# Optimization experiments

Hardware: AMD Instinct MI355X
Metric: run time of the kernel (lower is better)

The kernel has to match this reference:

```python
import jax, jax.numpy as jnp
import numpy as np

B, N, H = 512, 100, 768
I = 2 * H  # intermediate_dim default = hidden_dim * 2
NUM_ANS = 16
MAX_ANS = 15
LN_EPS = 1e-5


def setup_inputs() -> dict:
    key = jax.random.key(0)
    ks = jax.random.split(key, 7)
    s = 0.02
    return {
        "v_emb": jax.random.normal(ks[0], (B, N, H), dtype=jnp.float32),
        "W1": jax.random.normal(ks[1], (H, I), dtype=jnp.float32) * s,
        "b1": jax.random.normal(ks[2], (I,), dtype=jnp.float32) * s,
        "gamma": jnp.ones((I,), dtype=jnp.float32),
        "beta": jnp.zeros((I,), dtype=jnp.float32),
        "W2": jax.random.normal(ks[3], (I, 1), dtype=jnp.float32) * s,
        "b2": jax.random.normal(ks[4], (1,), dtype=jnp.float32) * s,
    }


def reference(v_emb, W1, b1, gamma, beta, W2, b2):
    # Linear -> GELU (exact/erf, torch nn.GELU default) -> LayerNorm -> Linear
    h = jnp.einsum("bnh,hi->bni", v_emb, W1) + b1            # [B,N,I]
    h = jax.nn.gelu(h, approximate=False)
    mu = jnp.mean(h, axis=-1, keepdims=True)
    var = jnp.mean(jnp.square(h - mu), axis=-1, keepdims=True)
    h = (h - mu) * jax.lax.rsqrt(var + LN_EPS) * gamma + beta
    scores = jnp.einsum("bni,io->bno", h, W2) + b2           # [B,N,1]
    scores = jax.nn.sigmoid(scores)                           # sigmoid=True branch
    pred = jnp.sum(scores, axis=1)                            # [B,1]
    # pred_to_logits: vectorized round + clamp + one-hot scatter
    # str(int(round(p))) in {'0'..'15'} -> that id; negative -> 0; overflow -> max_ans
    aid = jnp.clip(jnp.round(pred[:, 0]).astype(jnp.int32), 0, MAX_ANS)
    logits = jax.nn.one_hot(aid, NUM_ANS, dtype=scores.dtype)  # [B,16]
    # original returns dict: scores, final_attention_map (==scores), pred, logits
    return scores, pred, logits
```

## Files before the change

kernel.cpp:

```cpp
#include <hip/hip_runtime.h>
#include <hip/hip_bf16.h>
#include <cstdint>
#include <cstddef>

#define BB   512
#define NN   100
#define HH   768
#define II   1536
#define MM   (BB*NN)

typedef __bf16 bf16;
typedef __bf16 bf16x4 __attribute__((ext_vector_type(4)));
typedef __bf16 bf16x8 __attribute__((ext_vector_type(8)));
typedef float  f32x4  __attribute__((ext_vector_type(4)));

__device__ __forceinline__ void gld_lds16(const bf16* g, bf16* l) {
    __builtin_amdgcn_global_load_lds(
        (const __attribute__((address_space(1))) void*)g,
        (__attribute__((address_space(3))) void*)l, 16, 0, 0);
}

__device__ __forceinline__ float fast_gelu(float x) {
    const float ax = fabsf(x) * 0.70710678118654752f;
    const float t  = __builtin_amdgcn_rcpf(fmaf(0.3275911f, ax, 1.0f));
    float p = fmaf(1.061405429f, t, -1.453152027f);
    p = fmaf(p, t, 1.421413741f);
    p = fmaf(p, t, -0.284496736f);
    p = fmaf(p, t, 0.254829592f);
    p = p * t;
    const float e    = __expf(-ax * ax);
    const float erfa = fmaf(-p, e, 1.0f);
    const float erfx = copysignf(erfa, x);
    return 0.5f * x * (1.0f + erfx);
}

__global__ __launch_bounds__(256) void prep_kernel(
    const float* __restrict__ W1, const float* __restrict__ gamma,
    const float* __restrict__ beta, const float* __restrict__ W2,
    const float* __restrict__ b2,
    bf16* __restrict__ Wp, float* __restrict__ gw, float* __restrict__ scal)
{
    int bid = blockIdx.x;
    if (bid < 1152) {
        int t  = bid * 256 + threadIdx.x;
        int n  = t % II;
        int k0 = (t / II) * 4;
        bf16x4 v;
        v[0] = (bf16)W1[(size_t)(k0+0)*II + n];
        v[1] = (bf16)W1[(size_t)(k0+1)*II + n];
        v[2] = (bf16)W1[(size_t)(k0+2)*II + n];
        v[3] = (bf16)W1[(size_t)(k0+3)*II + n];
        *(bf16x4*)&Wp[(size_t)n*HH + k0] = v;
    } else if (bid == 1152) {
        for (int j = threadIdx.x; j < II; j += 256)
            gw[j] = gamma[j] * W2[j];
    } else {
        float s1 = 0.f, s2 = 0.f;
        for (int j = threadIdx.x; j < II; j += 256) {
            float w2 = W2[j];
            s1 += gamma[j] * w2;
            s2 += beta[j]  * w2;
        }
        #pragma unroll
        for (int off = 32; off; off >>= 1) {
            s1 += __shfl_down(s1, off, 64);
            s2 += __shfl_down(s2, off, 64);
        }
        __shared__ float a1[4], a2[4];
        int lane = threadIdx.x & 63, w = threadIdx.x >> 6;
        if (lane == 0) { a1[w] = s1; a2[w] = s2; }
        __syncthreads();
        if (threadIdx.x == 0) {
            scal[0] = a1[0] + a1[1] + a1[2] + a1[3];
            scal[1] = a2[0] + a2[1] + a2[2] + a2[3] + b2[0];
        }
    }
}

__global__ __launch_bounds__(256) void conv_kernel(
    const float* __restrict__ A, bf16* __restrict__ Apk)
{
    const size_t i = ((size_t)blockIdx.x * 256 + threadIdx.x) * 4;
    float4 v = *(const float4*)&A[i];
    bf16x4 o = { (bf16)v.x, (bf16)v.y, (bf16)v.z, (bf16)v.w };
    *(bf16x4*)&Apk[i] = o;
}

__global__ __launch_bounds__(256) void gemm_part(
    const bf16* __restrict__ Apk, const bf16* __restrict__ Wp,
    const float* __restrict__ b1, const float* __restrict__ gw,
    float* __restrict__ part)
{
    __shared__ bf16  As[128 * 64];
    __shared__ bf16  Bs[128 * 64];
    __shared__ float sred[2][128][3];

    const int tid  = threadIdx.x;
    const int lin  = (blockIdx.x % 8) * 600 + blockIdx.x / 8;
    const int mb   = lin / 12;
    const int nb   = lin % 12;
    const int lane = tid & 63;
    const int w    = tid >> 6;
    const int wm   = w >> 1;
    const int wn   = w & 1;
    const int m15  = lane & 15;
    const int q    = lane >> 4;
    const int row0 = mb * 128;

    const int rsub = tid >> 3;
    const int kgA  = (tid & 7) ^ (rsub & 7);
    const size_t gbase = (size_t)rsub * HH + (size_t)kgA * 8;
    const int    lbase = tid * 8;

    const bf16* Ag = Apk + (size_t)row0 * HH;
    const bf16* Bg = Wp  + (size_t)(nb * 128) * HH;

    f32x4 acc[4][4] = {};

    for (int kt = 0; kt < 12; ++kt) {
        const int koff = kt * 64;
        #pragma unroll
        for (int it = 0; it < 4; ++it) {
            size_t go = gbase + (size_t)it * 32 * HH + koff;
            int    lo = lbase + it * 2048;
            gld_lds16(Ag + go, &As[lo]);
            gld_lds16(Bg + go, &Bs[lo]);
        }
        asm volatile("s_waitcnt vmcnt(0)" ::: "memory");
        __syncthreads();

        #pragma unroll
        for (int kb = 0; kb < 2; ++kb) {
            const int swz = (((kb * 4 + q) ^ (m15 & 7)) * 8);
            bf16x8 af[4], bfr[4];
            #pragma unroll
            for (int mt = 0; mt < 4; ++mt)
                af[mt] = *(const bf16x8*)&As[(wm*64 + mt*16 + m15) * 64 + swz];
            #pragma unroll
            for (int nt = 0; nt < 4; ++nt)
                bfr[nt] = *(const bf16x8*)&Bs[(wn*64 + nt*16 + m15) * 64 + swz];
            #pragma unroll
            for (int mt = 0; mt < 4; ++mt)
                #pragma unroll
                for (int nt = 0; nt < 4; ++nt)
                    acc[mt][nt] = __builtin_amdgcn_mfma_f32_16x16x32_bf16(
                        af[mt], bfr[nt], acc[mt][nt], 0, 0, 0);
        }
        __syncthreads();
    }

    float bv[4], gv[4];
    #pragma unroll
    for (int nt = 0; nt < 4; ++nt) {
        const int col = nb*128 + wn*64 + nt*16 + m15;
        bv[nt] = b1[col];
        gv[nt] = gw[col];
    }

    #pragma unroll
    for (int mt = 0; mt < 4; ++mt) {
        #pragma unroll
        for (int r = 0; r < 4; ++r) {
            float x0 = 0.f, x1 = 0.f, x2 = 0.f;
            #pragma unroll
            for (int nt = 0; nt < 4; ++nt) {
                float g = fast_gelu(acc[mt][nt][r] + bv[nt]);
                x0 += g; x1 += g * g; x2 += g * gv[nt];
            }
            #pragma unroll
            for (int off = 8; off; off >>= 1) {
                x0 += __shfl_down(x0, off, 16);
                x1 += __shfl_down(x1, off, 16);
                x2 += __shfl_down(x2, off, 16);
            }
            if (m15 == 0) {
                const int rl = wm*64 + mt*16 + q*4 + r;
                sred[wn][rl][0] = x0;
                sred[wn][rl][1] = x1;
                sred[wn][rl][2] = x2;
            }
        }
    }
    __syncthreads();

    if (tid < 128) {
        const size_t rg = (size_t)row0 + tid;
        #pragma unroll
        for (int s = 0; s < 3; ++s)
            part[(size_t)s * 12 * MM + (size_t)nb * MM + rg]
                = sred[0][tid][s] + sred[1][tid][s];
    }
}

__global__ __launch_bounds__(128) void score_pred(
    const float* __restrict__ part, const float* __restrict__ scal,
    float* __restrict__ o_scores, float* __restrict__ o_pred,
    float* __restrict__ o_logits)
{
    const int b = blockIdx.x, t = threadIdx.x;
    float s = 0.f;
    if (t < NN) {
        const size_t row = (size_t)b * NN + t;
        float Sh = 0.f, Shh = 0.f, Shg = 0.f;
        #pragma unroll
        for (int j = 0; j < 12; ++j) {
            Sh  += part[(size_t)0*12*MM + (size_t)j*MM + row];
            Shh += part[(size_t)1*12*MM + (size_t)j*MM + row];
            Shg += part[(size_t)2*12*MM + (size_t)j*MM + row];
        }
        const float mu   = Sh * (1.0f / II);
        const float var  = Shh * (1.0f / II) - mu * mu;
        const float rstd = rsqrtf(var + 1e-5f);
        const float z    = rstd * (Shg - mu * scal[0]) + scal[1];
        s = 1.0f / (1.0f + __expf(-z));
        o_scores[row] = s;
    }
    float v = s;
    #pragma unroll
    for (int off = 32; off; off >>= 1) v += __shfl_down(v, off, 64);
    __shared__ float ssum[2];
    const int lane = t & 63, w = t >> 6;
    if (lane == 0) ssum[w] = v;
    __syncthreads();
    const float p = ssum[0] + ssum[1];
    if (t == 0) o_pred[b] = p;
    if (t < 16) {
        int aid = (int)rintf(p);
        aid = aid < 0 ? 0 : (aid > 15 ? 15 : aid);
        o_logits[b * 16 + t] = (t == aid) ? 1.0f : 0.0f;
    }
}

extern "C" void kernel_launch(void* const* d_in, const int* in_sizes, int n_in,
                              void* d_out, int out_size, void* d_ws, size_t ws_size,
                              hipStream_t stream)
{
    const float* v_emb = (const float*)d_in[0];
    const float* W1    = (const float*)d_in[1];
    const float* b1    = (const float*)d_in[2];
    const float* gamma = (const float*)d_in[3];
    const float* beta  = (const float*)d_in[4];
    const float* W2    = (const float*)d_in[5];
    const float* b2    = (const float*)d_in[6];

    char* ws = (char*)d_ws;
    size_t off = 0;
    bf16*  Wp   = (bf16*)(ws + off);  off += (size_t)II * HH * 2;
    float* gw   = (float*)(ws + off); off += (size_t)II * 4;
    float* scal = (float*)(ws + off); off += 256;
    float* part = (float*)(ws + off); off += (size_t)MM * 36 * 4;
    bf16*  Apk  = (bf16*)(ws + off);

    float* out       = (float*)d_out;
    float* o_scores  = out;
    float* o_pred    = out + MM;
    float* o_logits  = out + MM + BB;

    hipLaunchKernelGGL(prep_kernel, dim3(1154), dim3(256), 0, stream,
                       W1, gamma, beta, W2, b2, Wp, gw, scal);
    hipLaunchKernelGGL(conv_kernel, dim3((MM * HH) / (256 * 4)), dim3(256),
                       0, stream, v_emb, Apk);
    hipLaunchKernelGGL(gemm_part, dim3((MM / 128) * 12), dim3(256),
                       0, stream, Apk, Wp, b1, gw, part);
    hipLaunchKernelGGL(score_pred, dim3(BB), dim3(128), 0, stream,
                       part, scal, o_scores, o_pred, o_logits);
}
```

Baseline: 429.0 us.

## Fuse fp32-to-bf16 conversion of activations into GEMM tile loads

Drops the separate conversion kernel. The GEMM now reads fp32 v_emb directly, converts it to bf16 in registers and writes it to LDS, while the weight tile still goes through direct global-to-LDS loads. This removes a full pass that wrote and re-read the bf16 activation copy. The cost is that A is re-read as fp32 by each of the 12 N-blocks (twice the bytes per tile) and the load goes through VGPRs. It also replaces the 16-lane shuffle reduction with ds_swizzle butterflies.

```diff
diff --git a/kernel.cpp b/kernel.cpp
--- a/kernel.cpp
+++ b/kernel.cpp
@@ -18,6 +18,19 @@
     __builtin_amdgcn_global_load_lds(
         (const __attribute__((address_space(1))) void*)g,
         (__attribute__((address_space(3))) void*)l, 16, 0, 0);
+}
+
+template <int PAT>
+__device__ __forceinline__ float swz_add(float x) {
+    return x + __int_as_float(
+        __builtin_amdgcn_ds_swizzle(__float_as_int(x), PAT));
+}
+__device__ __forceinline__ float red16(float x) {
+    x = swz_add<0x041F>(x);
+    x = swz_add<0x081F>(x);
+    x = swz_add<0x101F>(x);
+    x = swz_add<0x201F>(x);
+    return x;
 }
 
 __device__ __forceinline__ float fast_gelu(float x) {
@@ -77,17 +90,8 @@
     }
 }
 
-__global__ __launch_bounds__(256) void conv_kernel(
-    const float* __restrict__ A, bf16* __restrict__ Apk)
-{
-    const size_t i = ((size_t)blockIdx.x * 256 + threadIdx.x) * 4;
-    float4 v = *(const float4*)&A[i];
-    bf16x4 o = { (bf16)v.x, (bf16)v.y, (bf16)v.z, (bf16)v.w };
-    *(bf16x4*)&Apk[i] = o;
-}
-
 __global__ __launch_bounds__(256) void gemm_part(
-    const bf16* __restrict__ Apk, const bf16* __restrict__ Wp,
+    const float* __restrict__ Af, const bf16* __restrict__ Wp,
     const float* __restrict__ b1, const float* __restrict__ gw,
     float* __restrict__ part)
 {
@@ -108,23 +112,26 @@
     const int row0 = mb * 128;
 
     const int rsub = tid >> 3;
-    const int kgA  = (tid & 7) ^ (rsub & 7);
-    const size_t gbase = (size_t)rsub * HH + (size_t)kgA * 8;
-    const int    lbase = tid * 8;
-
-    const bf16* Ag = Apk + (size_t)row0 * HH;
-    const bf16* Bg = Wp  + (size_t)(nb * 128) * HH;
+    const int kg   = (tid & 7) ^ (rsub & 7);
+    const int lbase = tid * 8;
+
+    const float* aP = Af + (size_t)(row0    + rsub) * HH + kg * 8;
+    const bf16*  bP = Wp + (size_t)(nb*128 + rsub) * HH + kg * 8;
 
     f32x4 acc[4][4] = {};
 
     for (int kt = 0; kt < 12; ++kt) {
-        const int koff = kt * 64;
+        #pragma unroll
+        for (int it = 0; it < 4; ++it)
+            gld_lds16(bP + (size_t)it * 32 * HH, &Bs[lbase + it * 2048]);
         #pragma unroll
         for (int it = 0; it < 4; ++it) {
-            size_t go = gbase + (size_t)it * 32 * HH + koff;
-            int    lo = lbase + it * 2048;
-            gld_lds16(Ag + go, &As[lo]);
-            gld_lds16(Bg + go, &Bs[lo]);
+            const float* s = aP + (size_t)it * 32 * HH;
+            float4 v0 = *(const float4*)(s);
+            float4 v1 = *(const float4*)(s + 4);
+            bf16x8 o = { (bf16)v0.x, (bf16)v0.y, (bf16)v0.z, (bf16)v0.w,
+                         (bf16)v1.x, (bf16)v1.y, (bf16)v1.z, (bf16)v1.w };
+            *(bf16x8*)&As[lbase + it * 2048] = o;
         }
         asm volatile("s_waitcnt vmcnt(0)" ::: "memory");
         __syncthreads();
@@ -147,6 +154,7 @@
                         af[mt], bfr[nt], acc[mt][nt], 0, 0, 0);
         }
         __syncthreads();
+        aP += 64; bP += 64;
     }
 
     float bv[4], gv[4];
@@ -167,12 +175,7 @@
                 float g = fast_gelu(acc[mt][nt][r] + bv[nt]);
                 x0 += g; x1 += g * g; x2 += g * gv[nt];
             }
-            #pragma unroll
-            for (int off = 8; off; off >>= 1) {
-                x0 += __shfl_down(x0, off, 16);
-                x1 += __shfl_down(x1, off, 16);
-                x2 += __shfl_down(x2, off, 16);
-            }
+            x0 = red16(x0); x1 = red16(x1); x2 = red16(x2);
             if (m15 == 0) {
                 const int rl = wm*64 + mt*16 + q*4 + r;
                 sred[wn][rl][0] = x0;
@@ -249,7 +252,6 @@
     float* gw   = (float*)(ws + off); off += (size_t)II * 4;
     float* scal = (float*)(ws + off); off += 256;
     float* part = (float*)(ws + off); off += (size_t)MM * 36 * 4;
-    bf16*  Apk  = (bf16*)(ws + off);
 
     float* out       = (float*)d_out;
     float* o_scores  = out;
@@ -258,10 +260,8 @@
 
     hipLaunchKernelGGL(prep_kernel, dim3(1154), dim3(256), 0, stream,
                        W1, gamma, beta, W2, b2, Wp, gw, scal);
-    hipLaunchKernelGGL(conv_kernel, dim3((MM * HH) / (256 * 4)), dim3(256),
-                       0, stream, v_emb, Apk);
     hipLaunchKernelGGL(gemm_part, dim3((MM / 128) * 12), dim3(256),
-                       0, stream, Apk, Wp, b1, gw, part);
+                       0, stream, v_emb, Wp, b1, gw, part);
     hipLaunchKernelGGL(score_pred, dim3(BB), dim3(128), 0, stream,
                        part, scal, o_scores, o_pred, o_logits);
 }
```

Result: faster. 394.0 us (-8.2%).
